# Kernel tuning notes

Measured on AMD Instinct MI355X. Metric: run time of the kernel, lower is better.

## Reference

```python
import jax, jax.numpy as jnp
import numpy as np

B, T, I, H, L, O = 64, 512, 128, 1024, 4, 128


def setup_inputs() -> dict:
    key = jax.random.key(0)
    ks = jax.random.split(key, 12)
    s_in = 1.0 / np.sqrt(H)  # PyTorch RNN init scale
    inp = {
        "x": jax.random.normal(ks[0], (B, T, I), jnp.float32),
        "hidden": jax.random.normal(ks[1], (L, B, H), jnp.float32) * 0.1,
        # layer 0 weights (input_size -> hidden)
        "W_ih0": jax.random.uniform(ks[2], (H, I), jnp.float32, -s_in, s_in),
        "W_hh0": jax.random.uniform(ks[3], (H, H), jnp.float32, -s_in, s_in),
        "b_ih0": jax.random.uniform(ks[4], (H,), jnp.float32, -s_in, s_in),
        "b_hh0": jax.random.uniform(ks[5], (H,), jnp.float32, -s_in, s_in),
        # layers 1..L-1 (hidden -> hidden), stacked
        "W_ih": jax.random.uniform(ks[6], (L - 1, H, H), jnp.float32, -s_in, s_in),
        "W_hh": jax.random.uniform(ks[7], (L - 1, H, H), jnp.float32, -s_in, s_in),
        "b_ih": jax.random.uniform(ks[8], (L - 1, H), jnp.float32, -s_in, s_in),
        "b_hh": jax.random.uniform(ks[9], (L - 1, H), jnp.float32, -s_in, s_in),
        # output projection
        "W_fc": jax.random.uniform(ks[10], (O, H), jnp.float32, -s_in, s_in),
        "b_fc": jax.random.uniform(ks[11], (O,), jnp.float32, -s_in, s_in),
    }
    return inp


def _run_layer(xs, h0, Wih, Whh, bih, bhh):
    # xs: [B, T, D_in]; h0: [B, H]. PyTorch RNN (relu):
    # h_t = relu(x_t @ Wih^T + b_ih + h_{t-1} @ Whh^T + b_hh)
    # Input projection is time-parallel; only the recurrence is scanned.
    xin = jnp.einsum('btd,hd->bth', xs, Wih) + bih + bhh  # [B,T,H]
    def step(h, x_t):
        h = jax.nn.relu(x_t + h @ Whh.T)
        return h, h
    h_last, ys = jax.lax.scan(step, h0, jnp.swapaxes(xin, 0, 1))  # ys: [T,B,H]
    return jnp.swapaxes(ys, 0, 1), h_last


def reference(x, hidden, W_ih0, W_hh0, b_ih0, b_hh0, W_ih, W_hh, b_ih, b_hh, W_fc, b_fc):
    out, h0_last = _run_layer(x, hidden[0], W_ih0, W_hh0, b_ih0, b_hh0)
    h_lasts = [h0_last]
    for l in range(L - 1):
        out, h_l = _run_layer(out, hidden[l + 1], W_ih[l], W_hh[l], b_ih[l], b_hh[l])
        h_lasts.append(h_l)
    output = jnp.einsum('bth,oh->bto', out, W_fc) + b_fc  # [B,T,O]
    h_n = jnp.stack(h_lasts, axis=0)  # [L,B,H]
    return output, h_n
```

## Files before the change

kernel.cpp:

```cpp
#include <hip/hip_runtime.h>

#define B_ 64
#define T_ 512
#define I_ 128
#define H_ 1024
#define L_ 4
#define O_ 128
#define M_ (B_ * T_)
#define D_ 32

typedef __attribute__((ext_vector_type(8))) short bf16x8_t;
typedef __attribute__((ext_vector_type(4))) float f32x4_t;

__device__ __forceinline__ unsigned short f2bf(float x) {
  unsigned int u = __builtin_bit_cast(unsigned int, x);
  u += 0x7FFFu + ((u >> 16) & 1u);
  return (unsigned short)(u >> 16);
}
__device__ __forceinline__ float bf2f(unsigned short h) {
  return __builtin_bit_cast(float, ((unsigned int)h) << 16);
}
__device__ __forceinline__ f32x4_t mfma16(bf16x8_t a, bf16x8_t b, f32x4_t c) {
  return __builtin_amdgcn_mfma_f32_16x16x32_bf16(a, b, c, 0, 0, 0);
}

__device__ __forceinline__ unsigned aldc(const unsigned* p) {
  return __hip_atomic_load(p, __ATOMIC_RELAXED, __HIP_MEMORY_SCOPE_AGENT);
}
__device__ __forceinline__ unsigned long long ald64(const unsigned long long* p) {
  return __hip_atomic_load(p, __ATOMIC_RELAXED, __HIP_MEMORY_SCOPE_AGENT);
}
__device__ __forceinline__ void ast32(unsigned* p, unsigned v) {
  __hip_atomic_store(p, v, __ATOMIC_RELAXED, __HIP_MEMORY_SCOPE_AGENT);
}

__device__ __forceinline__ unsigned wait_ge(const unsigned* base, unsigned target) {
  const int i = threadIdx.x & 15;
  unsigned v;
  while (true) {
    v = aldc(base + i * 32);
    if (__ballot(v < target) == 0ull) break;
    __builtin_amdgcn_s_sleep(2);
  }
  unsigned mn = v;
  mn = min(mn, (unsigned)__shfl_xor((int)mn, 1));
  mn = min(mn, (unsigned)__shfl_xor((int)mn, 2));
  mn = min(mn, (unsigned)__shfl_xor((int)mn, 4));
  mn = min(mn, (unsigned)__shfl_xor((int)mn, 8));
  return mn;
}

__device__ __forceinline__ void wait_all(const unsigned* base, unsigned target) {
  const int i = threadIdx.x & 15;
  while (true) {
    unsigned v = aldc(base + i * 32);
    if (__ballot(v < target) == 0ull) break;
    __builtin_amdgcn_s_sleep(2);
  }
}

template <int K, int N, bool ASPLIT, bool OUTBF16>
__global__ __launch_bounds__(256, 2) void gemm_k(
    const void* __restrict__ Aq, const float* __restrict__ Wf,
    const float* __restrict__ bias1, const float* __restrict__ bias2,
    void* __restrict__ Cq) {
  extern __shared__ unsigned short smem[];
  unsigned short* Ahi = smem;
  unsigned short* Alo = Ahi + (ASPLIT ? 8192 : 0);
  unsigned short* Bhi = Alo + 8192;
  unsigned short* Blo = Bhi + 8192;

  const int tid = threadIdx.x;
  const int wave = tid >> 6, lane = tid & 63;
  const int wm = wave >> 1, wn = wave & 1;
  const int lm = lane & 15, lk = lane >> 4;
  const int m0 = blockIdx.y * 128, n0 = blockIdx.x * 128;

  f32x4_t acc[4][4] = {};

  for (int kc = 0; kc < K; kc += 64) {
    __syncthreads();
#pragma unroll
    for (int p = 0; p < 4; ++p) {
      int fl = p * 256 + tid;
      int row = fl & 127, ko = (fl >> 7) & 3, kit = fl >> 9;
      int kk = kc + kit * 32 + ko * 8;
      if (ASPLIT) {
        const float* src = (const float*)Aq + (size_t)(m0 + row) * K + kk;
        union { bf16x8_t s; unsigned short u[8]; } th, tl;
#pragma unroll
        for (int e = 0; e < 8; ++e) {
          float v = src[e];
          unsigned short h = f2bf(v);
          th.u[e] = (short)h;
          tl.u[e] = (short)f2bf(v - bf2f(h));
        }
        *(bf16x8_t*)(Ahi + (size_t)fl * 8) = th.s;
        *(bf16x8_t*)(Alo + (size_t)fl * 8) = tl.s;
      } else {
        const unsigned short* src = (const unsigned short*)Aq + (size_t)(m0 + row) * K + kk;
        *(bf16x8_t*)(Ahi + (size_t)fl * 8) = *(const bf16x8_t*)src;
      }
    }
#pragma unroll
    for (int p = 0; p < 4; ++p) {
      int fl = p * 256 + tid;
      int row = fl & 127, ko = (fl >> 7) & 3, kit = fl >> 9;
      int kk = kc + kit * 32 + ko * 8;
      const float* src = Wf + (size_t)(n0 + row) * K + kk;
      union { bf16x8_t s; unsigned short u[8]; } th, tl;
#pragma unroll
      for (int e = 0; e < 8; ++e) {
        float v = src[e];
        unsigned short h = f2bf(v);
        th.u[e] = (short)h;
        tl.u[e] = (short)f2bf(v - bf2f(h));
      }
      *(bf16x8_t*)(Bhi + (size_t)fl * 8) = th.s;
      *(bf16x8_t*)(Blo + (size_t)fl * 8) = tl.s;
    }
    __syncthreads();
#pragma unroll
    for (int kit = 0; kit < 2; ++kit) {
      bf16x8_t bhf[4], blf[4];
#pragma unroll
      for (int n = 0; n < 4; ++n) {
        int br = wn * 64 + n * 16 + lm;
        bhf[n] = *(const bf16x8_t*)(Bhi + ((size_t)(kit * 4 + lk) * 128 + br) * 8);
        blf[n] = *(const bf16x8_t*)(Blo + ((size_t)(kit * 4 + lk) * 128 + br) * 8);
      }
#pragma unroll
      for (int m = 0; m < 4; ++m) {
        int ar = wm * 64 + m * 16 + lm;
        bf16x8_t a = *(const bf16x8_t*)(Ahi + ((size_t)(kit * 4 + lk) * 128 + ar) * 8);
        bf16x8_t al;
        if (ASPLIT) al = *(const bf16x8_t*)(Alo + ((size_t)(kit * 4 + lk) * 128 + ar) * 8);
#pragma unroll
        for (int n = 0; n < 4; ++n) {
          acc[m][n] = mfma16(a, bhf[n], acc[m][n]);
          acc[m][n] = mfma16(a, blf[n], acc[m][n]);
          if (ASPLIT) acc[m][n] = mfma16(al, bhf[n], acc[m][n]);
        }
      }
    }
  }
#pragma unroll
  for (int n = 0; n < 4; ++n) {
    int col = n0 + wn * 64 + n * 16 + lm;
    float bv = bias1[col];
    if (bias2 != nullptr) bv += bias2[col];
#pragma unroll
    for (int m = 0; m < 4; ++m) {
#pragma unroll
      for (int r = 0; r < 4; ++r) {
        int row = m0 + wm * 64 + m * 16 + lk * 4 + r;
        float v = acc[m][n][r] + bv;
        if (OUTBF16)
          ((unsigned short*)Cq)[(size_t)row * N + col] = f2bf(v);
        else
          ((float*)Cq)[(size_t)row * N + col] = v;
      }
    }
  }
}

__global__ __launch_bounds__(256) void splitx_k(const float* __restrict__ x,
                                               unsigned short* __restrict__ xhi,
                                               unsigned short* __restrict__ xlo) {
  int i = (blockIdx.x * 256 + threadIdx.x) * 4;
  float4 v = *(const float4*)(x + i);
  ushort4 h, lo;
  h.x = f2bf(v.x); lo.x = f2bf(v.x - bf2f(h.x));
  h.y = f2bf(v.y); lo.y = f2bf(v.y - bf2f(h.y));
  h.z = f2bf(v.z); lo.z = f2bf(v.z - bf2f(h.z));
  h.w = f2bf(v.w); lo.w = f2bf(v.w - bf2f(h.w));
  *(ushort4*)(xhi + i) = h;
  *(ushort4*)(xlo + i) = lo;
}

__global__ __launch_bounds__(256, 1) void rnn_k(
    const float* __restrict__ hidden,
    const float* __restrict__ Wih0, const float* __restrict__ Whh0,
    const float* __restrict__ bih0, const float* __restrict__ bhh0,
    const float* __restrict__ WihL, const float* __restrict__ WhhL,
    const float* __restrict__ bihL, const float* __restrict__ bhhL,
    const unsigned short* __restrict__ xhi, const unsigned short* __restrict__ xlo,
    unsigned short* __restrict__ ring, unsigned short* __restrict__ seqr,
    unsigned short* __restrict__ s3, float* __restrict__ hn,
    unsigned* __restrict__ prog) {
  extern __shared__ char lds[];
  char* ldsH = lds;
  char* ldsS = lds + 32768;
  const int tid = threadIdx.x;
  const int wave = tid >> 6, lane = tid & 63;
  const int lm = lane & 15, lk = lane >> 4;
  const int bid = blockIdx.x;
  const int l = bid >> 6;
  const int sub = bid & 63;
  const int me = sub >> 2, bg = sub & 3;
  const int g = l * 4 + bg;
  const int j0 = me * 64 + wave * 16;
  const int j = j0 + lm;

  const float* Whh = (l == 0) ? Whh0 : WhhL + (size_t)(l - 1) * H_ * H_;
  bf16x8_t bh[32];
#pragma unroll
  for (int kit = 0; kit < 32; ++kit) {
    const float* src = Whh + (size_t)j * H_ + kit * 32 + lk * 8;
    union { bf16x8_t s; unsigned short u[8]; } th;
#pragma unroll
    for (int e = 0; e < 8; ++e) th.u[e] = (short)f2bf(src[e]);
    bh[kit] = th.s;
  }
  bf16x8_t bw[32];
  bf16x8_t w0h[4], w0l[4];
  if (l > 0) {
    const float* Wih = WihL + (size_t)(l - 1) * H_ * H_;
#pragma unroll
    for (int kit = 0; kit < 32; ++kit) {
      const float* src = Wih + (size_t)j * H_ + kit * 32 + lk * 8;
      union { bf16x8_t s; unsigned short u[8]; } th;
#pragma unroll
      for (int e = 0; e < 8; ++e) th.u[e] = (short)f2bf(src[e]);
      bw[kit] = th.s;
    }
  } else {
#pragma unroll
    for (int kit = 0; kit < 4; ++kit) {
      const float* src = Wih0 + (size_t)j * I_ + kit * 32 + lk * 8;
      union { bf16x8_t s; unsigned short u[8]; } th, tl;
#pragma unroll
      for (int e = 0; e < 8; ++e) {
        float v = src[e];
        unsigned short h = f2bf(v);
        th.u[e] = (short)h;
        tl.u[e] = (short)f2bf(v - bf2f(h));
      }
      w0h[kit] = th.s; w0l[kit] = tl.s;
    }
  }
  float bias = (l == 0) ? (bih0[j] + bhh0[j])
                        : (bihL[(size_t)(l - 1) * H_ + j] + bhhL[(size_t)(l - 1) * H_ + j]);

  {
    unsigned* r1 = (unsigned*)(ring + ((size_t)(l * 2 + 1) * 4 + bg) * 16384);
#pragma unroll
    for (int q = 0; q < 2; ++q) {
      int s = q * 256 + tid;
      int J = s >> 6, b16 = (s >> 2) & 15, h4 = s & 3;
      int jj = me * 64 + J * 8 + h4 * 2;
      const float* hp = hidden + (size_t)l * B_ * H_ + (bg * 16 + b16) * H_ + jj;
      unsigned p0 = f2bf(hp[0]), p1 = f2bf(hp[1]);
      ast32(r1 + me * 512 + s, p0 | (p1 << 16));
    }
  }
  __syncthreads();
  if (tid == 0) ast32(prog + (size_t)(g * 16 + me) * 32, 1u);

  const unsigned* ownB = prog + (size_t)g * 512;
  const unsigned* upB = prog + (size_t)((l - 1) * 4 + bg) * 512;
  const unsigned* dnB = prog + (size_t)((l + 1) * 4 + bg) * 512;
  unsigned upMin = 1, dnMin = 1;
  f32x4_t a3s = {0.f, 0.f, 0.f, 0.f};

  auto precompute = [&](int tt) {
    if (l > 0) {
      if (upMin < (unsigned)(tt + 2)) upMin = wait_ge(upB, (unsigned)(tt + 2));
      asm volatile("" ::: "memory");
      unsigned long long stmp[16];
      const unsigned long long* sp = (const unsigned long long*)(seqr +
          ((size_t)((l - 1) * D_ + (tt & (D_ - 1))) * 4 + bg) * 16384);
#pragma unroll
      for (int i = 0; i < 16; ++i) stmp[i] = ald64(sp + i * 256 + tid);
      unsigned long long* dsp = (unsigned long long*)ldsS;
#pragma unroll
      for (int i = 0; i < 16; ++i) dsp[i * 256 + tid] = stmp[i];
      __syncthreads();
      f32x4_t xa = {0.f, 0.f, 0.f, 0.f}, xb = {0.f, 0.f, 0.f, 0.f};
#pragma unroll
      for (int kit = 0; kit < 32; ++kit) {
        const int fo = ((kit * 4 + lk) * 16 + lm) * 16;
        bf16x8_t as = *(const bf16x8_t*)(ldsS + fo);
        if (kit & 1) xb = mfma16(as, bw[kit], xb);
        else         xa = mfma16(as, bw[kit], xa);
      }
      a3s = xa + xb;
    } else {
      const int b = bg * 16 + lm;
      f32x4_t xa = {0.f, 0.f, 0.f, 0.f}, xb = {0.f, 0.f, 0.f, 0.f};
#pragma unroll
      for (int kit = 0; kit < 4; ++kit) {
        const size_t xo = ((size_t)b * T_ + tt) * I_ + kit * 32 + lk * 8;
        bf16x8_t xh = *(const bf16x8_t*)(xhi + xo);
        bf16x8_t xl = *(const bf16x8_t*)(xlo + xo);
        xa = mfma16(xh, w0h[kit], xa);
        xb = mfma16(xl, w0h[kit], xb);
        xa = mfma16(xh, w0l[kit], xa);
      }
      a3s = xa + xb;
    }
  };

  precompute(0);

  for (int t = 0; t < T_; ++t) {
    if (l < 3 && t >= D_) {
      if (dnMin < (unsigned)(t - D_ + 2)) dnMin = wait_ge(dnB, (unsigned)(t - D_ + 2));
    }
    wait_all(ownB, (unsigned)(t + 1));
    asm volatile("" ::: "memory");
    unsigned long long htmp[16];
    const unsigned long long* hp = (const unsigned long long*)(ring +
        ((size_t)(l * 2 + ((t & 1) ^ 1)) * 4 + bg) * 16384);
#pragma unroll
    for (int i = 0; i < 16; ++i) htmp[i] = ald64(hp + i * 256 + tid);
    {
      unsigned long long* dh = (unsigned long long*)ldsH;
#pragma unroll
      for (int i = 0; i < 16; ++i) dh[i * 256 + tid] = htmp[i];
    }
    __syncthreads();
    f32x4_t h0a = {0.f, 0.f, 0.f, 0.f}, h0b = {0.f, 0.f, 0.f, 0.f};
#pragma unroll
    for (int kit = 0; kit < 32; ++kit) {
      const int fo = ((kit * 4 + lk) * 16 + lm) * 16;
      bf16x8_t ah = *(const bf16x8_t*)(ldsH + fo);
      if (kit & 1) h0b = mfma16(ah, bh[kit], h0b);
      else         h0a = mfma16(ah, bh[kit], h0a);
    }
    unsigned* rwu = (unsigned*)(ring + ((size_t)(l * 2 + (t & 1)) * 4 + bg) * 16384);
    unsigned* swu = (unsigned*)(seqr + ((size_t)(l * D_ + (t & (D_ - 1))) * 4 + bg) * 16384);
    unsigned hi4[4];
#pragma unroll
    for (int r = 0; r < 4; ++r) {
      const int b15 = lk * 4 + r;
      float v = h0a[r] + h0b[r] + a3s[r] + bias;
      v = fmaxf(v, 0.f);
      unsigned hi = f2bf(v);
      hi4[r] = hi;
      unsigned other = (unsigned)__shfl_xor((int)hi, 1);
      if (!(lm & 1)) {
        const unsigned pk = hi | (other << 16);
        const int p32 = ((j >> 3) * 16 + b15) * 4 + ((j & 7) >> 1);
        ast32(rwu + p32, pk);
        if (l < 3) ast32(swu + p32, pk);
      }
      if (t == T_ - 1) hn[(size_t)l * B_ * H_ + (bg * 16 + b15) * H_ + j] = v;
    }
    __syncthreads();
    if (tid == 0) ast32(prog + (size_t)(g * 16 + me) * 32, (unsigned)(t + 2));
    if (l == 3) {
#pragma unroll
      for (int r = 0; r < 4; ++r)
        s3[((size_t)(bg * 16 + lk * 4 + r) * T_ + t) * H_ + j] = (unsigned short)hi4[r];
    }
    if (t + 1 < T_) precompute(t + 1);
  }
}

extern "C" void kernel_launch(void* const* d_in, const int* in_sizes, int n_in,
                              void* d_out, int out_size, void* d_ws, size_t ws_size,
                              hipStream_t stream) {
  const float* x = (const float*)d_in[0];
  const float* hidden = (const float*)d_in[1];
  const float* Wih0 = (const float*)d_in[2];
  const float* Whh0 = (const float*)d_in[3];
  const float* bih0 = (const float*)d_in[4];
  const float* bhh0 = (const float*)d_in[5];
  const float* WihL = (const float*)d_in[6];
  const float* WhhL = (const float*)d_in[7];
  const float* bihL = (const float*)d_in[8];
  const float* bhhL = (const float*)d_in[9];
  const float* Wfc = (const float*)d_in[10];
  const float* bfc = (const float*)d_in[11];
  float* out = (float*)d_out;
  float* hn = out + (size_t)M_ * O_;

  char* ws = (char*)d_ws;
  unsigned* prog = (unsigned*)ws;
  unsigned short* ring = (unsigned short*)(ws + 65536);
  unsigned short* seqr = (unsigned short*)(ws + 65536 + (1u << 20));
  unsigned short* s3 = (unsigned short*)(ws + 65536 + (1u << 20) + (12u << 20));
  unsigned short* xhi = (unsigned short*)(ws + 65536 + (1u << 20) + (12u << 20) + (64u << 20));
  unsigned short* xlo = xhi + (size_t)B_ * T_ * I_;

  hipMemsetAsync(ws, 0, 65536, stream);
  splitx_k<<<(B_ * T_ * I_) / 1024, 256, 0, stream>>>(x, xhi, xlo);

  hipFuncSetAttribute((const void*)rnn_k, hipFuncAttributeMaxDynamicSharedMemorySize,
                      64 * 1024);
  rnn_k<<<256, 256, 64 * 1024, stream>>>(hidden, Wih0, Whh0, bih0, bhh0,
                                         WihL, WhhL, bihL, bhhL, xhi, xlo,
                                         ring, seqr, s3, hn, prog);

  gemm_k<H_, O_, false, false><<<dim3(O_ / 128, M_ / 128), 256, 48 * 1024, stream>>>(
      (const void*)s3, Wfc, bfc, nullptr, (void*)out);
}
```

Baseline: 1.950 ms.

## Prefetch recurrent and input tiles early and overlap waits with MFMA chains

Splits the per-step precompute into gather and finish phases. The next step's input/sequence tile is issued before the barrier, and the hidden-state ring is loaded speculatively whenever a progress snapshot shows peers are already done. The downstream wait moves after the recurrent MFMA loop, and MFMA accumulation now uses four independent chains instead of two to shorten dependency latency. The goal is to hide global-load and spin-wait latency on the serial recurrence critical path. In exchange it costs more registers and adds synchronisation logic whose correctness depends on snapshot timing.

```diff
diff --git a/kernel.cpp b/kernel.cpp
--- a/kernel.cpp
+++ b/kernel.cpp
@@ -47,6 +47,8 @@
   mn = min(mn, (unsigned)__shfl_xor((int)mn, 2));
   mn = min(mn, (unsigned)__shfl_xor((int)mn, 4));
   mn = min(mn, (unsigned)__shfl_xor((int)mn, 8));
+  mn = min(mn, (unsigned)__shfl_xor((int)mn, 16));
+  mn = min(mn, (unsigned)__shfl_xor((int)mn, 32));
   return mn;
 }
 
@@ -262,79 +264,112 @@
   const unsigned* dnB = prog + (size_t)((l + 1) * 4 + bg) * 512;
   unsigned upMin = 1, dnMin = 1;
   f32x4_t a3s = {0.f, 0.f, 0.f, 0.f};
-
-  auto precompute = [&](int tt) {
+  unsigned long long htmp[16];
+  unsigned long long stmp[16];
+  bf16x8_t xh4[4], xl4[4];
+  bool hPre = false, sPre = false;
+  unsigned snap = 0;
+
+  auto gatherH = [&](int tt) {
+    const unsigned long long* hp = (const unsigned long long*)(ring +
+        ((size_t)(l * 2 + ((tt & 1) ^ 1)) * 4 + bg) * 16384);
+#pragma unroll
+    for (int i = 0; i < 16; ++i) htmp[i] = ald64(hp + i * 256 + tid);
+  };
+  auto gatherSeq = [&](int tt) {
+    const unsigned long long* sp = (const unsigned long long*)(seqr +
+        ((size_t)((l - 1) * D_ + (tt & (D_ - 1))) * 4 + bg) * 16384);
+#pragma unroll
+    for (int i = 0; i < 16; ++i) stmp[i] = ald64(sp + i * 256 + tid);
+  };
+  auto gatherX = [&](int tt) {
+    const int b = bg * 16 + lm;
+#pragma unroll
+    for (int kit = 0; kit < 4; ++kit) {
+      const size_t xo = ((size_t)b * T_ + tt) * I_ + kit * 32 + lk * 8;
+      xh4[kit] = *(const bf16x8_t*)(xhi + xo);
+      xl4[kit] = *(const bf16x8_t*)(xlo + xo);
+    }
+  };
+
+  auto finishPre = [&](int tt) {
     if (l > 0) {
-      if (upMin < (unsigned)(tt + 2)) upMin = wait_ge(upB, (unsigned)(tt + 2));
-      asm volatile("" ::: "memory");
-      unsigned long long stmp[16];
-      const unsigned long long* sp = (const unsigned long long*)(seqr +
-          ((size_t)((l - 1) * D_ + (tt & (D_ - 1))) * 4 + bg) * 16384);
-#pragma unroll
-      for (int i = 0; i < 16; ++i) stmp[i] = ald64(sp + i * 256 + tid);
+      if (!sPre) {
+        if (upMin < (unsigned)(tt + 2)) upMin = wait_ge(upB, (unsigned)(tt + 2));
+        asm volatile("" ::: "memory");
+        gatherSeq(tt);
+      }
       unsigned long long* dsp = (unsigned long long*)ldsS;
 #pragma unroll
       for (int i = 0; i < 16; ++i) dsp[i * 256 + tid] = stmp[i];
       __syncthreads();
-      f32x4_t xa = {0.f, 0.f, 0.f, 0.f}, xb = {0.f, 0.f, 0.f, 0.f};
+    }
+    hPre = (__ballot(snap < (unsigned)(tt + 1)) == 0ull);
+    asm volatile("" ::: "memory");
+    if (hPre) gatherH(tt);
+    if (l > 0) {
+      f32x4_t x0 = {0.f,0.f,0.f,0.f}, x1 = {0.f,0.f,0.f,0.f};
+      f32x4_t x2 = {0.f,0.f,0.f,0.f}, x3 = {0.f,0.f,0.f,0.f};
 #pragma unroll
       for (int kit = 0; kit < 32; ++kit) {
         const int fo = ((kit * 4 + lk) * 16 + lm) * 16;
         bf16x8_t as = *(const bf16x8_t*)(ldsS + fo);
-        if (kit & 1) xb = mfma16(as, bw[kit], xb);
-        else         xa = mfma16(as, bw[kit], xa);
-      }
-      a3s = xa + xb;
+        if ((kit & 3) == 0)      x0 = mfma16(as, bw[kit], x0);
+        else if ((kit & 3) == 1) x1 = mfma16(as, bw[kit], x1);
+        else if ((kit & 3) == 2) x2 = mfma16(as, bw[kit], x2);
+        else                     x3 = mfma16(as, bw[kit], x3);
+      }
+      a3s = (x0 + x1) + (x2 + x3);
     } else {
-      const int b = bg * 16 + lm;
-      f32x4_t xa = {0.f, 0.f, 0.f, 0.f}, xb = {0.f, 0.f, 0.f, 0.f};
+      f32x4_t x0 = {0.f,0.f,0.f,0.f}, x1 = {0.f,0.f,0.f,0.f}, x2 = {0.f,0.f,0.f,0.f};
 #pragma unroll
       for (int kit = 0; kit < 4; ++kit) {
-        const size_t xo = ((size_t)b * T_ + tt) * I_ + kit * 32 + lk * 8;
-        bf16x8_t xh = *(const bf16x8_t*)(xhi + xo);
-        bf16x8_t xl = *(const bf16x8_t*)(xlo + xo);
-        xa = mfma16(xh, w0h[kit], xa);
-        xb = mfma16(xl, w0h[kit], xb);
-        xa = mfma16(xh, w0l[kit], xa);
-      }
-      a3s = xa + xb;
+        x0 = mfma16(xh4[kit], w0h[kit], x0);
+        x1 = mfma16(xl4[kit], w0h[kit], x1);
+        x2 = mfma16(xh4[kit], w0l[kit], x2);
+      }
+      a3s = (x0 + x1) + x2;
     }
   };
 
-  precompute(0);
+  snap = aldc(ownB + (tid & 15) * 32);
+  sPre = false;
+  if (l == 0) { gatherX(0); sPre = true; }
+  finishPre(0);
 
   for (int t = 0; t < T_; ++t) {
-    if (l < 3 && t >= D_) {
-      if (dnMin < (unsigned)(t - D_ + 2)) dnMin = wait_ge(dnB, (unsigned)(t - D_ + 2));
-    }
-    wait_all(ownB, (unsigned)(t + 1));
-    asm volatile("" ::: "memory");
-    unsigned long long htmp[16];
-    const unsigned long long* hp = (const unsigned long long*)(ring +
-        ((size_t)(l * 2 + ((t & 1) ^ 1)) * 4 + bg) * 16384);
-#pragma unroll
-    for (int i = 0; i < 16; ++i) htmp[i] = ald64(hp + i * 256 + tid);
+    if (!hPre) {
+      wait_all(ownB, (unsigned)(t + 1));
+      asm volatile("" ::: "memory");
+      gatherH(t);
+    }
     {
       unsigned long long* dh = (unsigned long long*)ldsH;
 #pragma unroll
       for (int i = 0; i < 16; ++i) dh[i * 256 + tid] = htmp[i];
     }
     __syncthreads();
-    f32x4_t h0a = {0.f, 0.f, 0.f, 0.f}, h0b = {0.f, 0.f, 0.f, 0.f};
+    f32x4_t h0 = {0.f,0.f,0.f,0.f}, h1 = {0.f,0.f,0.f,0.f};
+    f32x4_t h2 = {0.f,0.f,0.f,0.f}, h3 = {0.f,0.f,0.f,0.f};
 #pragma unroll
     for (int kit = 0; kit < 32; ++kit) {
       const int fo = ((kit * 4 + lk) * 16 + lm) * 16;
       bf16x8_t ah = *(const bf16x8_t*)(ldsH + fo);
-      if (kit & 1) h0b = mfma16(ah, bh[kit], h0b);
-      else         h0a = mfma16(ah, bh[kit], h0a);
-    }
+      if ((kit & 3) == 0)      h0 = mfma16(ah, bh[kit], h0);
+      else if ((kit & 3) == 1) h1 = mfma16(ah, bh[kit], h1);
+      else if ((kit & 3) == 2) h2 = mfma16(ah, bh[kit], h2);
+      else                     h3 = mfma16(ah, bh[kit], h3);
+    }
+    f32x4_t a0 = (h0 + h1) + (h2 + h3);
+    if (l < 3 && t >= D_ && dnMin < (unsigned)(t - D_ + 2))
+      dnMin = wait_ge(dnB, (unsigned)(t - D_ + 2));
     unsigned* rwu = (unsigned*)(ring + ((size_t)(l * 2 + (t & 1)) * 4 + bg) * 16384);
     unsigned* swu = (unsigned*)(seqr + ((size_t)(l * D_ + (t & (D_ - 1))) * 4 + bg) * 16384);
     unsigned hi4[4];
 #pragma unroll
     for (int r = 0; r < 4; ++r) {
       const int b15 = lk * 4 + r;
-      float v = h0a[r] + h0b[r] + a3s[r] + bias;
+      float v = a0[r] + a3s[r] + bias;
       v = fmaxf(v, 0.f);
       unsigned hi = f2bf(v);
       hi4[r] = hi;
@@ -347,14 +382,23 @@
       }
       if (t == T_ - 1) hn[(size_t)l * B_ * H_ + (bg * 16 + b15) * H_ + j] = v;
     }
+    sPre = false;
+    if (t + 1 < T_) {
+      if (l > 0) {
+        if (upMin >= (unsigned)(t + 3)) { gatherSeq(t + 1); sPre = true; }
+      } else {
+        gatherX(t + 1); sPre = true;
+      }
+    }
     __syncthreads();
     if (tid == 0) ast32(prog + (size_t)(g * 16 + me) * 32, (unsigned)(t + 2));
+    snap = aldc(ownB + (tid & 15) * 32);
     if (l == 3) {
 #pragma unroll
       for (int r = 0; r < 4; ++r)
         s3[((size_t)(bg * 16 + lk * 4 + r) * T_ + t) * H_ + j] = (unsigned short)hi4[r];
     }
-    if (t + 1 < T_) precompute(t + 1);
+    if (t + 1 < T_) finishPre(t + 1);
   }
 }
 
```

Result: slower. 2.603 ms (+33.4%).
